# Optimization experiments

Measured on AMD Instinct MI355X. Metric: run time of the kernel, lower is better.

The kernel has to match this reference:

```python
import jax, jax.numpy as jnp
import numpy as np
from jax import lax

B, C, D, H, W = 2, 1, 128, 128, 128
CONSCIOUSNESS_WEIGHT = 0.1


def _field(depth, height, width, dtype):
    # sin(2*pi*(d+h+w)/(D+H+W)) broadcast over batch/channel
    d = jnp.arange(depth, dtype=dtype)[:, None, None]
    h = jnp.arange(height, dtype=dtype)[None, :, None]
    w = jnp.arange(width, dtype=dtype)[None, None, :]
    phase = 2.0 * jnp.pi * (d + h + w) / (depth + height + width)
    return jnp.sin(phase)  # [D,H,W]


def _conv3d(x, w, b):
    y = lax.conv_general_dilated(
        x, w, window_strides=(1, 1, 1), padding='SAME',
        dimension_numbers=('NCDHW', 'OIDHW', 'NCDHW'))
    return y + b[None, :, None, None, None]


def setup_inputs() -> dict:
    key = jax.random.key(0)
    ks = jax.random.split(key, 4)
    fan1 = 1 * 27
    fan2 = 8 * 27
    fan3 = 16 * 27
    return {
        'cube_data': jax.random.normal(ks[0], (B, C, D, H, W), dtype=jnp.float32),
        'w1': jax.random.normal(ks[1], (8, 1, 3, 3, 3), dtype=jnp.float32) / np.sqrt(fan1),
        'b1': jnp.zeros((8,), dtype=jnp.float32),
        'w2': jax.random.normal(ks[2], (16, 8, 3, 3, 3), dtype=jnp.float32) / np.sqrt(fan2),
        'b2': jnp.zeros((16,), dtype=jnp.float32),
        'w3': jax.random.normal(ks[3], (1, 16, 3, 3, 3), dtype=jnp.float32) / np.sqrt(fan3),
        'b3': jnp.zeros((1,), dtype=jnp.float32),
    }


def reference(cube_data, w1, b1, w2, b2, w3, b3):
    _, _, d, h, w = cube_data.shape
    field = _field(d, h, w, cube_data.dtype)[None, None]  # [1,1,D,H,W]
    integrated = cube_data * (1.0 + CONSCIOUSNESS_WEIGHT * field)
    x = jax.nn.relu(_conv3d(integrated, w1, b1))
    x = jax.nn.relu(_conv3d(x, w2, b2))
    x = jnp.tanh(_conv3d(x, w3, b3))
    return x
```

## Files before the change

### kernel.cpp

```cpp
#include <hip/hip_runtime.h>
#include <hip/hip_fp16.h>

#define VOX (128 * 128 * 128)
#define P 130
#define PP (P * P)
#define PVOX (P * P * P)
#define LROW 130
#define PLANE (6 * LROW)

typedef unsigned short u16;
typedef _Float16 f16x2 __attribute__((ext_vector_type(2)));
typedef _Float16 f16x8 __attribute__((ext_vector_type(8)));
typedef __attribute__((ext_vector_type(4))) float f32x4;
typedef __attribute__((ext_vector_type(2))) float f32x2;

__device__ __forceinline__ u16 f2h(float f) {
    return __builtin_bit_cast(unsigned short, (_Float16)f);
}
__device__ __forceinline__ unsigned pkh_relu(float a, float b) {
    float ra = a > 0.f ? a : 0.f, rb = b > 0.f ? b : 0.f;
    return (unsigned)f2h(ra) | ((unsigned)f2h(rb) << 16);
}
__device__ __forceinline__ f16x2 h2(unsigned u) { return __builtin_bit_cast(f16x2, u); }

__device__ __forceinline__ float dot2(unsigned a, unsigned b, float c) {
#if __has_builtin(__builtin_amdgcn_fdot2)
    return __builtin_amdgcn_fdot2(h2(a), h2(b), c, false);
#else
    f16x2 av = h2(a), bv = h2(b);
    c = fmaf((float)av.x, (float)bv.x, c);
    return fmaf((float)av.y, (float)bv.y, c);
#endif
}

__device__ __forceinline__ float fast_tanh(float x) {
    float e = __expf(2.0f * x);
    return 1.0f - 2.0f * __builtin_amdgcn_rcpf(1.0f + e);
}

__device__ __forceinline__ void gload_lds16(const u16* g, u16* l) {
    __builtin_amdgcn_global_load_lds(
        (const __attribute__((address_space(1))) unsigned int*)g,
        (__attribute__((address_space(3))) unsigned int*)l,
        16, 0, 0);
}

__global__ __launch_bounds__(256) void integrate_kernel(
    const float* __restrict__ in, u16* __restrict__ x0,
    const float* __restrict__ w1, const float* __restrict__ w2,
    const float* __restrict__ w3, u16* __restrict__ w2frag,
    unsigned* __restrict__ w3p, float2* __restrict__ w1p,
    u16* __restrict__ x1, u16* __restrict__ x2) {
    int i = blockIdx.x * 256 + threadIdx.x;
    if (i < 3584) {
        int j = i & 7, l = (i >> 3) & 63, s = i >> 9;
        int tap = s * 4 + (l >> 4), oc = l & 15;
        float v = (tap < 27) ? w2[(oc * 8 + j) * 27 + tap] : 0.0f;
        w2frag[i] = f2h(v);
    }
    if (i < 216) {
        int tap = i >> 3, j = i & 7;
        w3p[i] = (unsigned)f2h(w3[(2 * j) * 27 + tap]) |
                 ((unsigned)f2h(w3[(2 * j + 1) * 27 + tap]) << 16);
    }
    if (i < 108) {
        int tap = i >> 2, j = i & 3;
        w1p[i] = make_float2(w1[(2 * j) * 27 + tap], w1[(2 * j + 1) * 27 + tap]);
    }
    if (i >= PVOX) return;
    int d = i / PP;
    int r = i - d * PP;
    int h = r / P;
    int w = r - h * P;
    const bool interior = (d >= 1 && d <= 128 && h >= 1 && h <= 128 && w >= 1 && w <= 128);
    float v = 0.0f;
    if (interior) {
        int s = (d - 1) + (h - 1) + (w - 1);
        float fld = 1.0f + 0.1f * sinf(6.283185307179586f * (float)s / 384.0f);
        v = in[(size_t)(d - 1) * 16384 + (h - 1) * 128 + (w - 1)] * fld;
    } else {
        uint4 z = {0u, 0u, 0u, 0u};
        *(uint4*)(x1 + (size_t)i * 8) = z;
        *(uint4*)(x2 + (size_t)i * 16) = z;
        *(uint4*)(x2 + (size_t)i * 16 + 8) = z;
    }
    x0[i] = f2h(v);
}

__global__ __launch_bounds__(256) void conv1_kernel(
    const u16* __restrict__ x0, const float2* __restrict__ w1p,
    const float* __restrict__ b1, u16* __restrict__ x1) {
    const int t = blockIdx.x * 256 + threadIdx.x;
    const int w0 = (t & 63) * 2;
    const int h0 = ((t >> 6) & 31) * 4;
    const int d = t >> 11;

    f32x2 acc[4][4][2];
#pragma unroll
    for (int j = 0; j < 4; ++j) {
        const f32x2 b = {b1[2 * j], b1[2 * j + 1]};
#pragma unroll
        for (int i = 0; i < 4; ++i) { acc[i][j][0] = b; acc[i][j][1] = b; }
    }

#pragma unroll
    for (int dz = 0; dz < 3; ++dz) {
        const u16* zb = x0 + (size_t)(d + dz) * PP + (size_t)h0 * P + w0;
        const float2* wz = w1p + dz * 9 * 4;
#pragma unroll
        for (int r = 0; r < 6; ++r) {
            const u16* rp = zb + r * P;
            const unsigned u0 = *(const unsigned*)rp;
            const unsigned u1 = *(const unsigned*)(rp + 2);
            float vv[4];
            vv[0] = (float)h2(u0).x; vv[1] = (float)h2(u0).y;
            vv[2] = (float)h2(u1).x; vv[3] = (float)h2(u1).y;
#pragma unroll
            for (int dy = 0; dy < 3; ++dy) {
                const int i = r - dy;
                if (i < 0 || i > 3) continue;
#pragma unroll
                for (int dx = 0; dx < 3; ++dx) {
                    const f32x2 s0 = {vv[dx], vv[dx]};
                    const f32x2 s1 = {vv[dx + 1], vv[dx + 1]};
#pragma unroll
                    for (int j = 0; j < 4; ++j) {
                        const float2 wraw = wz[(dy * 3 + dx) * 4 + j];
                        const f32x2 wv = {wraw.x, wraw.y};
                        acc[i][j][0] = __builtin_elementwise_fma(wv, s0, acc[i][j][0]);
                        acc[i][j][1] = __builtin_elementwise_fma(wv, s1, acc[i][j][1]);
                    }
                }
            }
        }
    }
    const size_t e0 = ((size_t)(d + 1) * P + (h0 + 1)) * P + (w0 + 1);
#pragma unroll
    for (int i = 0; i < 4; ++i) {
        uint4 oA, oB;
        oA.x = pkh_relu(acc[i][0][0].x, acc[i][0][0].y);
        oA.y = pkh_relu(acc[i][1][0].x, acc[i][1][0].y);
        oA.z = pkh_relu(acc[i][2][0].x, acc[i][2][0].y);
        oA.w = pkh_relu(acc[i][3][0].x, acc[i][3][0].y);
        oB.x = pkh_relu(acc[i][0][1].x, acc[i][0][1].y);
        oB.y = pkh_relu(acc[i][1][1].x, acc[i][1][1].y);
        oB.z = pkh_relu(acc[i][2][1].x, acc[i][2][1].y);
        oB.w = pkh_relu(acc[i][3][1].x, acc[i][3][1].y);
        *(uint4*)(x1 + (e0 + (size_t)i * P) * 8) = oA;
        *(uint4*)(x1 + (e0 + (size_t)i * P + 1) * 8) = oB;
    }
}

__global__ __launch_bounds__(256) void conv2_mfma_kernel(
    const u16* __restrict__ x1, const u16* __restrict__ w2frag,
    const float* __restrict__ b2, u16* __restrict__ x2) {
    __shared__ u16 sm[4 * PLANE * 8];

    const int tid = threadIdx.x;
    const int lane = tid & 63;
    const int wv = tid >> 6;
    const int q = lane >> 4;
    const int mi = lane & 15;
    const int D0 = (blockIdx.x >> 5) * 8;
    const int h0 = (blockIdx.x & 31) * 4;

    f16x8 wf[7];
#pragma unroll
    for (int s = 0; s < 7; ++s)
        wf[s] = *(const f16x8*)(w2frag + (size_t)(s * 64 + lane) * 8);

#pragma unroll
    for (int p = 0; p < 3; ++p) {
        const int pd = D0 + p;
        const int slot = pd & 3;
        const u16* gb = x1 + ((size_t)(pd * P + h0) * P) * 8;
        u16* lb = sm + (size_t)slot * PLANE * 8;
#pragma unroll
        for (int k = 0; k < 3; ++k) {
            const int u0 = wv * 64 + k * 256;
            gload_lds16(gb + (size_t)(u0 + lane) * 8, lb + (size_t)u0 * 8);
        }
        if (wv == 0 && lane < PLANE - 768)
            gload_lds16(gb + (size_t)(768 + lane) * 8, lb + (size_t)768 * 8);
    }
    __syncthreads();

    const float4 bv = *(const float4*)(b2 + q * 4);

#pragma unroll 1
    for (int i = 0; i < 8; ++i) {
        const int dout = D0 + i;

        if (i < 7) {
            const int pd = dout + 3;
            const int slot = pd & 3;
            const u16* gb = x1 + ((size_t)(pd * P + h0) * P) * 8;
            u16* lb = sm + (size_t)slot * PLANE * 8;
#pragma unroll
            for (int k = 0; k < 3; ++k) {
                const int u0 = wv * 64 + k * 256;
                gload_lds16(gb + (size_t)(u0 + lane) * 8, lb + (size_t)u0 * 8);
            }
            if (wv == 0 && lane < PLANE - 768)
                gload_lds16(gb + (size_t)(768 + lane) * 8, lb + (size_t)768 * 8);
        }

        f32x4 acc[8];
#pragma unroll
        for (int t = 0; t < 8; ++t) acc[t] = (f32x4){0.f, 0.f, 0.f, 0.f};

#pragma unroll
        for (int s = 0; s < 7; ++s) {
            int tap = s * 4 + q;
            if (tap > 26) tap = 26;
            const int dz = tap / 9;
            const int rem = tap - dz * 9;
            const int dy = rem / 3;
            const int dx = rem - dy * 3;
            const int slot = (dout + dz) & 3;
            const u16* bp = sm + ((size_t)(slot * 6 + wv + dy) * LROW + (mi + dx)) * 8;
#pragma unroll
            for (int t = 0; t < 8; ++t) {
                f16x8 act = *(const f16x8*)(bp + t * 128);
                acc[t] = __builtin_amdgcn_mfma_f32_16x16x32_f16(wf[s], act, acc[t], 0, 0, 0);
            }
        }

        const size_t obase = ((size_t)(dout + 1) * P + (h0 + wv + 1)) * P + 1;
#pragma unroll
        for (int t = 0; t < 8; ++t) {
            uint2 o;
            o.x = pkh_relu(acc[t][0] + bv.x, acc[t][1] + bv.y);
            o.y = pkh_relu(acc[t][2] + bv.z, acc[t][3] + bv.w);
            *(uint2*)(x2 + (obase + 16 * t + mi) * 16 + q * 4) = o;
        }

        if (i < 7) __syncthreads();
    }
}

__global__ __launch_bounds__(256) void conv3_kernel(
    const u16* __restrict__ x2, const unsigned* __restrict__ w3p,
    const float* __restrict__ b3, float* __restrict__ out) {
    const int t = blockIdx.x * 256 + threadIdx.x;
    const int w = t & 127;
    const int h0 = ((t >> 7) & 31) * 4;
    const int d0 = (t >> 12) * 2;

    float accA[2][4], accB[2][4];
#pragma unroll
    for (int dd = 0; dd < 2; ++dd)
#pragma unroll
        for (int i = 0; i < 4; ++i) { accA[dd][i] = 0.f; accB[dd][i] = 0.f; }

#pragma unroll 1
    for (int z = 0; z < 4; ++z) {
        const u16* zb = x2 + ((size_t)((d0 + z) * P + h0) * P + w) * 16;
#pragma unroll
        for (int r = 0; r < 6; ++r) {
            const u16* rp = zb + (size_t)r * (P * 16);
            const uint4 c0l = *(const uint4*)(rp);
            const uint4 c0h = *(const uint4*)(rp + 8);
            const uint4 c1l = *(const uint4*)(rp + 16);
            const uint4 c1h = *(const uint4*)(rp + 24);
            const uint4 c2l = *(const uint4*)(rp + 32);
            const uint4 c2h = *(const uint4*)(rp + 40);
#pragma unroll
            for (int dd = 0; dd < 2; ++dd) {
                const int dz = z - dd;
                if (dz < 0 || dz > 2) continue;
                const unsigned* wz = w3p + dz * 9 * 8;
#pragma unroll
                for (int dy = 0; dy < 3; ++dy) {
                    const int i = r - dy;
                    if (i < 0 || i > 3) continue;
                    const unsigned* wp = wz + dy * 3 * 8;
                    float a = accA[dd][i], b = accB[dd][i];
                    a = dot2(c0l.x, wp[0], a);  b = dot2(c0l.y, wp[1], b);
                    a = dot2(c0l.z, wp[2], a);  b = dot2(c0l.w, wp[3], b);
                    a = dot2(c0h.x, wp[4], a);  b = dot2(c0h.y, wp[5], b);
                    a = dot2(c0h.z, wp[6], a);  b = dot2(c0h.w, wp[7], b);
                    a = dot2(c1l.x, wp[8], a);  b = dot2(c1l.y, wp[9], b);
                    a = dot2(c1l.z, wp[10], a); b = dot2(c1l.w, wp[11], b);
                    a = dot2(c1h.x, wp[12], a); b = dot2(c1h.y, wp[13], b);
                    a = dot2(c1h.z, wp[14], a); b = dot2(c1h.w, wp[15], b);
                    a = dot2(c2l.x, wp[16], a); b = dot2(c2l.y, wp[17], b);
                    a = dot2(c2l.z, wp[18], a); b = dot2(c2l.w, wp[19], b);
                    a = dot2(c2h.x, wp[20], a); b = dot2(c2h.y, wp[21], b);
                    a = dot2(c2h.z, wp[22], a); b = dot2(c2h.w, wp[23], b);
                    accA[dd][i] = a; accB[dd][i] = b;
                }
            }
        }
    }
    const float bias = b3[0];
#pragma unroll
    for (int dd = 0; dd < 2; ++dd) {
        const size_t obase = (size_t)((d0 + dd) * 128 + h0) * 128 + w;
#pragma unroll
        for (int i = 0; i < 4; ++i)
            out[obase + (size_t)i * 128] = fast_tanh(accA[dd][i] + accB[dd][i] + bias);
    }
}

extern "C" void kernel_launch(void* const* d_in, const int* in_sizes, int n_in,
                              void* d_out, int out_size, void* d_ws, size_t ws_size,
                              hipStream_t stream) {
    const float* cube = (const float*)d_in[0];
    const float* w1 = (const float*)d_in[1];
    const float* b1 = (const float*)d_in[2];
    const float* w2 = (const float*)d_in[3];
    const float* b2 = (const float*)d_in[4];
    const float* w3 = (const float*)d_in[5];
    const float* b3 = (const float*)d_in[6];
    float* out = (float*)d_out;

    char* ws = (char*)d_ws;
    u16* w2frag = (u16*)ws;
    unsigned* w3p = (unsigned*)(ws + 7168);
    float2* w1p = (float2*)(ws + 8032);
    u16* x0 = (u16*)(ws + 16384);
    u16* x1 = (u16*)(ws + 16384 + (size_t)PVOX * sizeof(u16));
    u16* x2 = (u16*)(ws + 16384 + (size_t)PVOX * sizeof(u16) + (size_t)PVOX * 8 * sizeof(u16));

    for (int b = 0; b < 2; ++b) {
        integrate_kernel<<<dim3((PVOX + 255) / 256), dim3(256), 0, stream>>>(
            cube + (size_t)b * VOX, x0, w1, w2, w3, w2frag, w3p, w1p, x1, x2);
        conv1_kernel<<<dim3(VOX / 8 / 256), dim3(256), 0, stream>>>(x0, w1p, b1, x1);
        conv2_mfma_kernel<<<dim3(512), dim3(256), 0, stream>>>(x1, w2frag, b2, x2);
        conv3_kernel<<<dim3(VOX / 8 / 256), dim3(256), 0, stream>>>(
            x2, w3p, b3, out + (size_t)b * VOX);
    }
}
```

Baseline: 219.9 us.

## Fuse field integration into conv1 and batch both samples per launch

Removes the separate integrate pass and its fp16 padded x0 buffer. conv1 now reads the fp32 input directly, applies the sine field per row using __sinf, and handles the halo with bounds checks. When the workspace is large enough, per-sample buffers are allocated so conv1 and conv3 cover both batch samples in one grid, and the halo zeroing runs once in a setup kernel. This cuts the launch count and removes one full-volume read/write pass. The cost is extra sin evaluations and branches in conv1, __sinf precision, and a fallback path that depends on ws_size.

```diff
diff --git a/kernel.cpp b/kernel.cpp
--- a/kernel.cpp
+++ b/kernel.cpp
@@ -45,12 +45,12 @@
         16, 0, 0);
 }
 
-__global__ __launch_bounds__(256) void integrate_kernel(
-    const float* __restrict__ in, u16* __restrict__ x0,
+__global__ __launch_bounds__(256) void setup_kernel(
     const float* __restrict__ w1, const float* __restrict__ w2,
     const float* __restrict__ w3, u16* __restrict__ w2frag,
     unsigned* __restrict__ w3p, float2* __restrict__ w1p,
-    u16* __restrict__ x1, u16* __restrict__ x2) {
+    u16* __restrict__ x1a, u16* __restrict__ x1b,
+    u16* __restrict__ x2a, u16* __restrict__ x2b, int nb) {
     int i = blockIdx.x * 256 + threadIdx.x;
     if (i < 3584) {
         int j = i & 7, l = (i >> 3) & 63, s = i >> 9;
@@ -73,28 +73,37 @@
     int h = r / P;
     int w = r - h * P;
     const bool interior = (d >= 1 && d <= 128 && h >= 1 && h <= 128 && w >= 1 && w <= 128);
-    float v = 0.0f;
-    if (interior) {
-        int s = (d - 1) + (h - 1) + (w - 1);
-        float fld = 1.0f + 0.1f * sinf(6.283185307179586f * (float)s / 384.0f);
-        v = in[(size_t)(d - 1) * 16384 + (h - 1) * 128 + (w - 1)] * fld;
-    } else {
+    if (!interior) {
         uint4 z = {0u, 0u, 0u, 0u};
-        *(uint4*)(x1 + (size_t)i * 8) = z;
-        *(uint4*)(x2 + (size_t)i * 16) = z;
-        *(uint4*)(x2 + (size_t)i * 16 + 8) = z;
-    }
-    x0[i] = f2h(v);
+        *(uint4*)(x1a + (size_t)i * 8) = z;
+        *(uint4*)(x2a + (size_t)i * 16) = z;
+        *(uint4*)(x2a + (size_t)i * 16 + 8) = z;
+        if (nb == 2) {
+            *(uint4*)(x1b + (size_t)i * 8) = z;
+            *(uint4*)(x2b + (size_t)i * 16) = z;
+            *(uint4*)(x2b + (size_t)i * 16 + 8) = z;
+        }
+    }
 }
 
 __global__ __launch_bounds__(256) void conv1_kernel(
-    const u16* __restrict__ x0, const float2* __restrict__ w1p,
-    const float* __restrict__ b1, u16* __restrict__ x1) {
+    const float* __restrict__ in0, const float2* __restrict__ w1p,
+    const float* __restrict__ b1, u16* __restrict__ x1a, u16* __restrict__ x1b) {
     const int t = blockIdx.x * 256 + threadIdx.x;
+    const float* in = in0 + (size_t)blockIdx.y * VOX;
+    u16* x1 = blockIdx.y ? x1b : x1a;
     const int w0 = (t & 63) * 2;
     const int h0 = ((t >> 6) & 31) * 4;
     const int d = t >> 11;
 
+    float fld[11];
+    {
+        const float s0 = (float)(d + h0 + w0 - 3);
+#pragma unroll
+        for (int k = 0; k < 11; ++k)
+            fld[k] = 1.0f + 0.1f * __sinf((s0 + (float)k) * 0.016362461737446838f);
+    }
+
     f32x2 acc[4][4][2];
 #pragma unroll
     for (int j = 0; j < 4; ++j) {
@@ -105,16 +114,23 @@
 
 #pragma unroll
     for (int dz = 0; dz < 3; ++dz) {
-        const u16* zb = x0 + (size_t)(d + dz) * PP + (size_t)h0 * P + w0;
+        const int di = d + dz - 1;
+        const bool dok = (unsigned)di < 128u;
+        const float* zb = in + (size_t)di * 16384 + (w0 - 1);
         const float2* wz = w1p + dz * 9 * 4;
 #pragma unroll
         for (int r = 0; r < 6; ++r) {
-            const u16* rp = zb + r * P;
-            const unsigned u0 = *(const unsigned*)rp;
-            const unsigned u1 = *(const unsigned*)(rp + 2);
-            float vv[4];
-            vv[0] = (float)h2(u0).x; vv[1] = (float)h2(u0).y;
-            vv[2] = (float)h2(u1).x; vv[3] = (float)h2(u1).y;
+            const int hi = h0 + r - 1;
+            const bool rok = dok && ((unsigned)hi < 128u);
+            const float* rp = zb + hi * 128;
+            float vv[4] = {0.f, 0.f, 0.f, 0.f};
+            if (rok) {
+                const float2 m = *(const float2*)(rp + 1);
+                vv[1] = m.x * fld[dz + r + 1];
+                vv[2] = m.y * fld[dz + r + 2];
+                if (w0 > 0)   vv[0] = rp[0] * fld[dz + r];
+                if (w0 < 126) vv[3] = rp[3] * fld[dz + r + 3];
+            }
 #pragma unroll
             for (int dy = 0; dy < 3; ++dy) {
                 const int i = r - dy;
@@ -240,9 +256,12 @@
 }
 
 __global__ __launch_bounds__(256) void conv3_kernel(
-    const u16* __restrict__ x2, const unsigned* __restrict__ w3p,
-    const float* __restrict__ b3, float* __restrict__ out) {
+    const u16* __restrict__ x2a, const u16* __restrict__ x2b,
+    const unsigned* __restrict__ w3p, const float* __restrict__ b3,
+    float* __restrict__ out0) {
     const int t = blockIdx.x * 256 + threadIdx.x;
+    const u16* x2 = blockIdx.y ? x2b : x2a;
+    float* out = out0 + (size_t)blockIdx.y * VOX;
     const int w = t & 127;
     const int h0 = ((t >> 7) & 31) * 4;
     const int d0 = (t >> 12) * 2;
@@ -319,16 +338,33 @@
     u16* w2frag = (u16*)ws;
     unsigned* w3p = (unsigned*)(ws + 7168);
     float2* w1p = (float2*)(ws + 8032);
-    u16* x0 = (u16*)(ws + 16384);
-    u16* x1 = (u16*)(ws + 16384 + (size_t)PVOX * sizeof(u16));
-    u16* x2 = (u16*)(ws + 16384 + (size_t)PVOX * sizeof(u16) + (size_t)PVOX * 8 * sizeof(u16));
-
-    for (int b = 0; b < 2; ++b) {
-        integrate_kernel<<<dim3((PVOX + 255) / 256), dim3(256), 0, stream>>>(
-            cube + (size_t)b * VOX, x0, w1, w2, w3, w2frag, w3p, w1p, x1, x2);
-        conv1_kernel<<<dim3(VOX / 8 / 256), dim3(256), 0, stream>>>(x0, w1p, b1, x1);
-        conv2_mfma_kernel<<<dim3(512), dim3(256), 0, stream>>>(x1, w2frag, b2, x2);
-        conv3_kernel<<<dim3(VOX / 8 / 256), dim3(256), 0, stream>>>(
-            x2, w3p, b3, out + (size_t)b * VOX);
-    }
-}
+    const size_t X1SZ = (size_t)PVOX * 16;
+    const size_t X2SZ = (size_t)PVOX * 32;
+
+    const bool dual = ws_size >= (size_t)16384 + 2 * X1SZ + 2 * X2SZ;
+
+    u16* x1a = (u16*)(ws + 16384);
+    u16* x1b = dual ? (u16*)(ws + 16384 + X1SZ) : x1a;
+    u16* x2a = (u16*)(ws + 16384 + (dual ? 2 : 1) * X1SZ);
+    u16* x2b = dual ? (u16*)((char*)x2a + X2SZ) : x2a;
+
+    setup_kernel<<<dim3((PVOX + 255) / 256), dim3(256), 0, stream>>>(
+        w1, w2, w3, w2frag, w3p, w1p, x1a, x1b, x2a, x2b, dual ? 2 : 1);
+
+    if (dual) {
+        conv1_kernel<<<dim3(VOX / 8 / 256, 2), dim3(256), 0, stream>>>(
+            cube, w1p, b1, x1a, x1b);
+        conv2_mfma_kernel<<<dim3(512), dim3(256), 0, stream>>>(x1a, w2frag, b2, x2a);
+        conv2_mfma_kernel<<<dim3(512), dim3(256), 0, stream>>>(x1b, w2frag, b2, x2b);
+        conv3_kernel<<<dim3(VOX / 8 / 256, 2), dim3(256), 0, stream>>>(
+            x2a, x2b, w3p, b3, out);
+    } else {
+        for (int b = 0; b < 2; ++b) {
+            conv1_kernel<<<dim3(VOX / 8 / 256, 1), dim3(256), 0, stream>>>(
+                cube + (size_t)b * VOX, w1p, b1, x1a, x1a);
+            conv2_mfma_kernel<<<dim3(512), dim3(256), 0, stream>>>(x1a, w2frag, b2, x2a);
+            conv3_kernel<<<dim3(VOX / 8 / 256, 1), dim3(256), 0, stream>>>(
+                x2a, x2a, w3p, b3, out + (size_t)b * VOX);
+        }
+    }
+}
```

Result: slower. 280.4 us (+27.5%).
